# Kernel optimization log

Measured on AMD Instinct MI355X. Metric: run time of the kernel, lower is better.

The kernel has to match this reference:

```python
import jax, jax.numpy as jnp
import numpy as np

EPS = 1e-6  # torch.nn.PairwiseDistance default eps: dist = ||x - y + eps||_2


def setup_inputs() -> dict:
    key = jax.random.key(0)
    k1, k2 = jax.random.split(key)
    samples = jax.random.normal(k1, (4096, 128), dtype=jnp.float32)   # batch of observations
    V = jax.random.uniform(k2, (65536, 128), dtype=jnp.float32)       # grown node codebook (torch.rand init)
    return {"samples": samples, "V": V}


def reference(samples, V):
    # activate_bmu, vectorized over the batch.
    # torch PairwiseDistance(p=2): d_n = || x - V_n + eps ||_2
    D = samples.shape[-1]
    x_sq = jnp.sum(samples * samples, axis=-1)        # [B]
    v_sq = jnp.sum(V * V, axis=-1)                    # [N]
    xv = jnp.einsum('bd,nd->bn', samples, V)          # [B, N]
    x_sum = jnp.sum(samples, axis=-1)                 # [B]
    v_sum = jnp.sum(V, axis=-1)                       # [N]
    sq = (x_sq[:, None] + v_sq[None, :] - 2.0 * xv
          + 2.0 * EPS * (x_sum[:, None] - v_sum[None, :]) + D * EPS * EPS)
    dists = jnp.sqrt(jnp.maximum(sq, 0.0))            # [B, N]
    # top-2 smallest distances -> BMU b, second BMU s
    neg_top2, idx = jax.lax.top_k(-dists, 2)          # [B, 2]
    b = idx[:, 0]
    s = idx[:, 1]
    a = jnp.exp(neg_top2[:, 0])                       # exp(-b_dist)
    return (b, s, a)
```

## Files before the change

kernel.cpp:

```cpp
#include <hip/hip_runtime.h>
#include <math.h>

#define NS 4096
#define NV 65536
#define DDIM 128
#define EPSV 1e-6f
#define NCHUNK 16
#define TILES_PER_CHUNK 32
#define FLTMAX 3.402823466e+38f
#define IMAX 0x7fffffff

#define XSQ_F    0
#define XSUM_F   4096
#define PART_F   8192
#define D12_F    139264
#define CNT_I    147456
#define CELL1_I  147472
#define CELL2_I  151568
#define BUCKET_I 155664
#define WS_TILED_BYTE 1605632
#define TILE_BYTES 65536
#define TILE_STRIDE 66560

typedef __attribute__((ext_vector_type(8)))  __bf16        bf16x8;
typedef __attribute__((ext_vector_type(8)))  unsigned short ush8;
typedef __attribute__((ext_vector_type(4)))  unsigned short ush4;
typedef __attribute__((ext_vector_type(16))) float          f32x16;

typedef const __attribute__((address_space(1))) unsigned int* gp_t;
typedef __attribute__((address_space(3))) unsigned int*       lp_t;

__device__ __forceinline__ void async_cp16(const void* g, void* l) {
    __builtin_amdgcn_global_load_lds((gp_t)g, (lp_t)l, 16, 0, 0);
}

__device__ __forceinline__ unsigned short f2bf(float x) {
    unsigned u = __builtin_bit_cast(unsigned, x);
    u += 0x7FFFu + ((u >> 16) & 1u);
    return (unsigned short)(u >> 16);
}
__device__ __forceinline__ float bf2f(unsigned short h) {
    unsigned u = ((unsigned)h) << 16;
    return __builtin_bit_cast(float, u);
}

__device__ __forceinline__ void stage_tile(const char* src, char* lds, int tid) {
    #pragma unroll
    for (int i = 0; i < 16; i++) {
        int off = (i * 256 + tid) * 16;
        async_cp16(src + off, lds + off);
    }
    if (tid < 64) {
        int off = TILE_BYTES + tid * 16;
        async_cp16(src + off, lds + off);
    }
}

__device__ __forceinline__ void load_bfrag(const float* __restrict__ samples,
                                           int srow, int q, ush8* bh, ush8* bl) {
    const float4* s4 = (const float4*)samples;
    #pragma unroll
    for (int s = 0; s < 8; s++) {
        float4 x0 = s4[(size_t)srow * 32 + s * 4 + q * 2];
        float4 x1 = s4[(size_t)srow * 32 + s * 4 + q * 2 + 1];
        float xs[8] = {x0.x, x0.y, x0.z, x0.w, x1.x, x1.y, x1.z, x1.w};
        #pragma unroll
        for (int j = 0; j < 8; j++) {
            float y = -2.0f * xs[j];
            unsigned short hh = f2bf(y);
            bh[s][j] = hh;
            bl[s][j] = f2bf(y - bf2f(hh));
        }
    }
}

__device__ __forceinline__ void tile_mfma(const char* lds, const ush8* bh, const ush8* bl,
                                          int q, int l31, f32x16 acc[4]) {
    #pragma unroll
    for (int mi = 0; mi < 4; mi++) {
        #pragma unroll
        for (int g = 0; g < 4; g++) {
            float4 cj = *(const float4*)(lds + TILE_BYTES + (size_t)(mi * 32 + g * 8 + 4 * q) * 4);
            acc[mi][g * 4 + 0] = cj.x;
            acc[mi][g * 4 + 1] = cj.y;
            acc[mi][g * 4 + 2] = cj.z;
            acc[mi][g * 4 + 3] = cj.w;
        }
    }
    #pragma unroll
    for (int s = 0; s < 8; s++) {
        bf16x8 bhs = __builtin_bit_cast(bf16x8, bh[s]);
        bf16x8 bls = __builtin_bit_cast(bf16x8, bl[s]);
        #pragma unroll
        for (int mi = 0; mi < 4; mi++) {
            bf16x8 ah = *(const bf16x8*)(lds + (size_t)((((s * 2 + 0) * 2 + q) * 128) + mi * 32 + l31) * 16);
            bf16x8 al = *(const bf16x8*)(lds + (size_t)((((s * 2 + 1) * 2 + q) * 128) + mi * 32 + l31) * 16);
            acc[mi] = __builtin_amdgcn_mfma_f32_32x32x16_bf16(ah, bhs, acc[mi], 0, 0, 0);
            acc[mi] = __builtin_amdgcn_mfma_f32_32x32x16_bf16(ah, bls, acc[mi], 0, 0, 0);
            acc[mi] = __builtin_amdgcn_mfma_f32_32x32x16_bf16(al, bhs, acc[mi], 0, 0, 0);
        }
    }
}

__global__ void vq_prep(const float* __restrict__ samples,
                        const float* __restrict__ V,
                        char* __restrict__ ws) {
    float* ws_f = (float*)ws;
    int* ws_i = (int*)ws;
    const int b = blockIdx.x;
    const int tid = threadIdx.x;
    if (b >= NV / 128) {
        if (b == NV / 128 && tid < NCHUNK) ws_i[CNT_I + tid] = 0;
        int row = (b - NV / 128) * 4 + (tid >> 6);
        int lane = tid & 63;
        float2 v = ((const float2*)(samples + (size_t)row * DDIM))[lane];
        float s = v.x + v.y;
        float q = v.x * v.x + v.y * v.y;
        #pragma unroll
        for (int off = 32; off >= 1; off >>= 1) {
            s += __shfl_xor(s, off);
            q += __shfl_xor(q, off);
        }
        if (lane == 0) { ws_f[XSQ_F + row] = q; ws_f[XSUM_F + row] = s; }
        return;
    }
    const int tile = b;
    char* dst = ws + WS_TILED_BYTE + (size_t)tile * TILE_STRIDE;
    const float4* v4 = (const float4*)V;
    #pragma unroll
    for (int i = 0; i < 16; i++) {
        int flat = i * 256 + tid;
        int row = flat >> 5;
        int kq = flat & 31;
        float4 g = v4[(size_t)(tile * 128 + row) * 32 + kq];
        float s = g.x + g.y + g.z + g.w;
        float q2 = g.x * g.x + g.y * g.y + g.z * g.z + g.w * g.w;
        #pragma unroll
        for (int off = 16; off >= 1; off >>= 1) {
            s += __shfl_xor(s, off);
            q2 += __shfl_xor(q2, off);
        }
        if ((tid & 31) == 0)
            *(float*)(dst + TILE_BYTES + row * 4) = q2 - 2.0f * EPSV * s;
        int k0 = kq * 4;
        int sI = k0 >> 4, qI = (k0 >> 3) & 1, j0 = k0 & 7;
        float xs[4] = {g.x, g.y, g.z, g.w};
        ush4 h, l;
        #pragma unroll
        for (int e = 0; e < 4; e++) {
            unsigned short hh = f2bf(xs[e]);
            h[e] = hh;
            l[e] = f2bf(xs[e] - bf2f(hh));
        }
        *(ush4*)(dst + ((((sI * 2 + 0) * 2 + qI) * 128) + row) * 16 + j0 * 2) = h;
        *(ush4*)(dst + ((((sI * 2 + 1) * 2 + qI) * 128) + row) * 16 + j0 * 2) = l;
    }
}

__global__ __launch_bounds__(256, 2)
void vq_gemm_topk(const float* __restrict__ samples, char* __restrict__ ws) {
    __shared__ __align__(16) char lds[TILE_STRIDE];
    const int tid = threadIdx.x;
    const int w = tid >> 6, lane = tid & 63;
    const int l31 = lane & 31, q = lane >> 5;
    const int st = blockIdx.x;
    const int chunk = blockIdx.y;
    const int nrow = st * 128 + w * 32 + l31;

    ush8 bh[8], bl[8];
    load_bfrag(samples, nrow, q, bh, bl);

    float rd1[4], rd2[4];
    #pragma unroll
    for (int mi = 0; mi < 4; mi++) { rd1[mi] = FLTMAX; rd2[mi] = FLTMAX; }

    const char* tile0 = ws + WS_TILED_BYTE + (size_t)(chunk * TILES_PER_CHUNK) * TILE_STRIDE;

    for (int it = 0; it < TILES_PER_CHUNK; it++) {
        stage_tile(tile0 + (size_t)it * TILE_STRIDE, lds, tid);
        __syncthreads();
        f32x16 acc[4];
        tile_mfma(lds, bh, bl, q, l31, acc);
        #pragma unroll
        for (int mi = 0; mi < 4; mi++) {
            #pragma unroll
            for (int r = 0; r < 16; r++) {
                float v = acc[mi][r];
                rd2[mi] = fminf(rd2[mi], fmaxf(rd1[mi], v));
                rd1[mi] = fminf(rd1[mi], v);
            }
        }
        __syncthreads();
    }

    float d1 = rd1[0], d2 = rd2[0];
    #pragma unroll
    for (int mi = 1; mi < 4; mi++) {
        float t = fmaxf(d1, rd1[mi]);
        d1 = fminf(d1, rd1[mi]);
        d2 = fminf(fminf(t, d2), rd2[mi]);
    }
    {
        float od1 = __shfl_xor(d1, 32), od2 = __shfl_xor(d2, 32);
        float t = fmaxf(d1, od1);
        d1 = fminf(d1, od1);
        d2 = fminf(fminf(t, d2), od2);
    }
    if (q == 0) {
        float2* part = (float2*)((float*)ws + PART_F);
        part[(size_t)nrow * NCHUNK + chunk] = make_float2(d1, d2);
    }
}

__global__ void vq_merge(float* __restrict__ ws_f, float* __restrict__ out) {
    const int m = blockIdx.x * 256 + threadIdx.x;
    const int lane = threadIdx.x & 63;
    int* ws_i = (int*)ws_f;
    const float2* part = (const float2*)(ws_f + PART_F);
    float2 p[NCHUNK];
    float g1 = FLTMAX, g2 = FLTMAX;
    #pragma unroll
    for (int c = 0; c < NCHUNK; c++) {
        p[c] = part[(size_t)m * NCHUNK + c];
        float t = fmaxf(g1, p[c].x);
        g1 = fminf(g1, p[c].x);
        g2 = fminf(fminf(t, g2), p[c].y);
    }
    ((float2*)(ws_f + D12_F))[m] = make_float2(g1, g2);
    ws_i[CELL1_I + m] = IMAX;
    ws_i[CELL2_I + m] = IMAX;
    float ci = ws_f[XSQ_F + m] + 2.0f * EPSV * ws_f[XSUM_F + m] + (float)DDIM * EPSV * EPSV;
    out[2 * NS + m] = expf(-sqrtf(fmaxf(ci + g1, 0.0f)));
    #pragma unroll
    for (int c = 0; c < NCHUNK; c++) {
        bool want = (p[c].x == g1) || (p[c].x == g2) || (p[c].y == g2);
        unsigned long long mk = __ballot(want);
        if (mk) {
            int leader = (int)__ffsll(mk) - 1;
            int base = 0;
            if (lane == leader) base = atomicAdd(&ws_i[CNT_I + c], (int)__popcll(mk));
            base = __shfl(base, leader);
            if (want) {
                int pos = base + (int)__popcll(mk & ((1ull << lane) - 1ull));
                ws_i[BUCKET_I + c * NS + pos] = m;
            }
        }
    }
}

__global__ __launch_bounds__(256, 2)
void vq_recover(const float* __restrict__ samples, char* __restrict__ ws) {
    __shared__ __align__(16) char lds[TILE_STRIDE];
    const int tid = threadIdx.x;
    const int w = tid >> 6, lane = tid & 63;
    const int l31 = lane & 31, q = lane >> 5;
    const int tg = blockIdx.x;
    const int chunk = blockIdx.z;
    int* ws_i = (int*)ws;
    float* ws_f = (float*)ws;
    const int cnt = ws_i[CNT_I + chunk];
    const char* tile0 = ws + WS_TILED_BYTE + (size_t)(chunk * TILES_PER_CHUNK) * TILE_STRIDE;

    for (int sy = blockIdx.y; sy * 128 < cnt; sy += 4) {
        int slot = sy * 128 + w * 32 + l31;
        bool valid = slot < cnt;
        int sample = valid ? ws_i[BUCKET_I + chunk * NS + slot] : 0;
        ush8 bh[8], bl[8];
        load_bfrag(samples, sample, q, bh, bl);
        float d1t, d2t;
        if (valid) {
            float2 dt = ((const float2*)(ws_f + D12_F))[sample];
            d1t = dt.x; d2t = dt.y;
        } else {
            d1t = __int_as_float(0x7fc00000);
            d2t = d1t;
        }
        #pragma unroll 1
        for (int it = tg * 4; it < tg * 4 + 4; it++) {
            stage_tile(tile0 + (size_t)it * TILE_STRIDE, lds, tid);
            __syncthreads();
            f32x16 acc[4];
            tile_mfma(lds, bh, bl, q, l31, acc);
            const int cbase = chunk * 4096 + it * 128 + 4 * q;
            #pragma unroll
            for (int mi = 0; mi < 4; mi++) {
                #pragma unroll
                for (int r = 0; r < 16; r++) {
                    float v = acc[mi][r];
                    if (v == d1t) {
                        int idx = cbase + mi * 32 + (r >> 2) * 8 + (r & 3);
                        int old = atomicMin(&ws_i[CELL1_I + sample], idx);
                        int loser = old > idx ? old : idx;
                        atomicMin(&ws_i[CELL2_I + sample], loser);
                    } else if (v == d2t) {
                        int idx = cbase + mi * 32 + (r >> 2) * 8 + (r & 3);
                        atomicMin(&ws_i[CELL2_I + sample], idx);
                    }
                }
            }
            __syncthreads();
        }
    }
}

__global__ void vq_finalize(const char* __restrict__ ws, float* __restrict__ out) {
    const int m = blockIdx.x * 256 + threadIdx.x;
    const int* ws_i = (const int*)ws;
    out[m]      = (float)ws_i[CELL1_I + m];
    out[NS + m] = (float)ws_i[CELL2_I + m];
}

extern "C" void kernel_launch(void* const* d_in, const int* in_sizes, int n_in,
                              void* d_out, int out_size, void* d_ws, size_t ws_size,
                              hipStream_t stream) {
    (void)in_sizes; (void)n_in; (void)out_size; (void)ws_size;
    const float* samples = (const float*)d_in[0];
    const float* V = (const float*)d_in[1];
    float* out = (float*)d_out;
    float* ws_f = (float*)d_ws;
    char*  ws_b = (char*)d_ws;

    vq_prep<<<dim3(NV / 128 + NS / 4), 256, 0, stream>>>(samples, V, ws_b);
    vq_gemm_topk<<<dim3(NS / 128, NCHUNK), 256, 0, stream>>>(samples, ws_b);
    vq_merge<<<dim3(NS / 256), 256, 0, stream>>>(ws_f, out);
    vq_recover<<<dim3(8, 4, NCHUNK), 256, 0, stream>>>(samples, ws_b);
    vq_finalize<<<dim3(NS / 256), 256, 0, stream>>>(ws_b, out);
}
```

Before: 341.9 us.

## Flip GEMM operands, track winning tile per sample, recover per tile

The main GEMM now stages the 128-sample block in LDS once and streams the codebook tiles directly from global memory into registers. This removes the per-tile LDS staging and the two barriers per iteration. The top-2 search also records which tile produced each candidate, so the recovery pass launches one block per tile and only recomputes for samples whose best or second-best fell in that tile, replacing the bucketed per-chunk atomic lists. The prep kernel transposes V through LDS so it can write 16-byte bf16 fragments, and the grid is remapped to group chunks. The risks are register pressure from per-iteration global loads without LDS reuse across waves, and extra index bookkeeping.

```diff
diff --git a/kernel.cpp b/kernel.cpp
--- a/kernel.cpp
+++ b/kernel.cpp
@@ -7,17 +7,17 @@
 #define EPSV 1e-6f
 #define NCHUNK 16
 #define TILES_PER_CHUNK 32
+#define NTILE 512
 #define FLTMAX 3.402823466e+38f
 #define IMAX 0x7fffffff
 
 #define XSQ_F    0
 #define XSUM_F   4096
 #define PART_F   8192
-#define D12_F    139264
-#define CNT_I    147456
-#define CELL1_I  147472
-#define CELL2_I  151568
-#define BUCKET_I 155664
+#define D12_F    270336
+#define T12_I    278528
+#define CELL1_I  286720
+#define CELL2_I  290816
 #define WS_TILED_BYTE 1605632
 #define TILE_BYTES 65536
 #define TILE_STRIDE 66560
@@ -27,13 +27,6 @@
 typedef __attribute__((ext_vector_type(4)))  unsigned short ush4;
 typedef __attribute__((ext_vector_type(16))) float          f32x16;
 
-typedef const __attribute__((address_space(1))) unsigned int* gp_t;
-typedef __attribute__((address_space(3))) unsigned int*       lp_t;
-
-__device__ __forceinline__ void async_cp16(const void* g, void* l) {
-    __builtin_amdgcn_global_load_lds((gp_t)g, (lp_t)l, 16, 0, 0);
-}
-
 __device__ __forceinline__ unsigned short f2bf(float x) {
     unsigned u = __builtin_bit_cast(unsigned, x);
     u += 0x7FFFu + ((u >> 16) & 1u);
@@ -44,60 +37,65 @@
     return __builtin_bit_cast(float, u);
 }
 
-__device__ __forceinline__ void stage_tile(const char* src, char* lds, int tid) {
-    #pragma unroll
-    for (int i = 0; i < 16; i++) {
-        int off = (i * 256 + tid) * 16;
-        async_cp16(src + off, lds + off);
-    }
-    if (tid < 64) {
-        int off = TILE_BYTES + tid * 16;
-        async_cp16(src + off, lds + off);
-    }
-}
-
-__device__ __forceinline__ void load_bfrag(const float* __restrict__ samples,
-                                           int srow, int q, ush8* bh, ush8* bl) {
-    const float4* s4 = (const float4*)samples;
+__device__ __forceinline__ void merge2t(float& d1, int& i1, float& d2, int& i2,
+                                        float d, int i) {
+    bool b1 = (d < d1) || (d == d1 && i < i1);
+    bool b2 = (d < d2) || (d == d2 && i < i2);
+    if (b1) { d2 = d1; i2 = i1; d1 = d; i1 = i; }
+    else if (b2) { d2 = d; i2 = i; }
+}
+
+__device__ __forceinline__ void cvt_sample_piece(const float4* __restrict__ s4,
+                                                 int srcrow, int row, int kq,
+                                                 char* lds) {
+    float4 xv = s4[(size_t)srcrow * 32 + kq];
+    int k0 = kq * 4, sI = k0 >> 4, qI = (k0 >> 3) & 1, j0 = k0 & 7;
+    float xs[4] = {xv.x, xv.y, xv.z, xv.w};
+    ush4 h, l;
+    #pragma unroll
+    for (int e = 0; e < 4; e++) {
+        float y = -2.0f * xs[e];
+        unsigned short hh = f2bf(y);
+        h[e] = hh;
+        l[e] = f2bf(y - bf2f(hh));
+    }
+    *(ush4*)(lds + ((((sI * 2 + 0) * 2 + qI) * 128) + row) * 16 + j0 * 2) = h;
+    *(ush4*)(lds + ((((sI * 2 + 1) * 2 + qI) * 128) + row) * 16 + j0 * 2) = l;
+}
+
+__device__ __forceinline__ void tile_mfma_flip(const char* __restrict__ tsrc,
+                                               const char* __restrict__ lds,
+                                               int w, int qb, int l31,
+                                               f32x16 acc[4]) {
+    ush8 ah[8], al[8];
     #pragma unroll
     for (int s = 0; s < 8; s++) {
-        float4 x0 = s4[(size_t)srow * 32 + s * 4 + q * 2];
-        float4 x1 = s4[(size_t)srow * 32 + s * 4 + q * 2 + 1];
-        float xs[8] = {x0.x, x0.y, x0.z, x0.w, x1.x, x1.y, x1.z, x1.w};
-        #pragma unroll
-        for (int j = 0; j < 8; j++) {
-            float y = -2.0f * xs[j];
-            unsigned short hh = f2bf(y);
-            bh[s][j] = hh;
-            bl[s][j] = f2bf(y - bf2f(hh));
-        }
-    }
-}
-
-__device__ __forceinline__ void tile_mfma(const char* lds, const ush8* bh, const ush8* bl,
-                                          int q, int l31, f32x16 acc[4]) {
-    #pragma unroll
-    for (int mi = 0; mi < 4; mi++) {
-        #pragma unroll
-        for (int g = 0; g < 4; g++) {
-            float4 cj = *(const float4*)(lds + TILE_BYTES + (size_t)(mi * 32 + g * 8 + 4 * q) * 4);
-            acc[mi][g * 4 + 0] = cj.x;
-            acc[mi][g * 4 + 1] = cj.y;
-            acc[mi][g * 4 + 2] = cj.z;
-            acc[mi][g * 4 + 3] = cj.w;
-        }
+        ah[s] = *(const ush8*)(tsrc + (size_t)((((s * 2 + 0) * 2 + qb) * 128) + w * 32 + l31) * 16);
+        al[s] = *(const ush8*)(tsrc + (size_t)((((s * 2 + 1) * 2 + qb) * 128) + w * 32 + l31) * 16);
+    }
+    const char* cjb = tsrc + TILE_BYTES + (size_t)(w * 32 + 4 * qb) * 4;
+    float4 cj0 = *(const float4*)(cjb);
+    float4 cj1 = *(const float4*)(cjb + 32);
+    float4 cj2 = *(const float4*)(cjb + 64);
+    float4 cj3 = *(const float4*)(cjb + 96);
+    #pragma unroll
+    for (int sg = 0; sg < 4; sg++) {
+        acc[sg][0] = cj0.x;  acc[sg][1] = cj0.y;  acc[sg][2] = cj0.z;  acc[sg][3] = cj0.w;
+        acc[sg][4] = cj1.x;  acc[sg][5] = cj1.y;  acc[sg][6] = cj1.z;  acc[sg][7] = cj1.w;
+        acc[sg][8] = cj2.x;  acc[sg][9] = cj2.y;  acc[sg][10] = cj2.z; acc[sg][11] = cj2.w;
+        acc[sg][12] = cj3.x; acc[sg][13] = cj3.y; acc[sg][14] = cj3.z; acc[sg][15] = cj3.w;
     }
     #pragma unroll
     for (int s = 0; s < 8; s++) {
-        bf16x8 bhs = __builtin_bit_cast(bf16x8, bh[s]);
-        bf16x8 bls = __builtin_bit_cast(bf16x8, bl[s]);
-        #pragma unroll
-        for (int mi = 0; mi < 4; mi++) {
-            bf16x8 ah = *(const bf16x8*)(lds + (size_t)((((s * 2 + 0) * 2 + q) * 128) + mi * 32 + l31) * 16);
-            bf16x8 al = *(const bf16x8*)(lds + (size_t)((((s * 2 + 1) * 2 + q) * 128) + mi * 32 + l31) * 16);
-            acc[mi] = __builtin_amdgcn_mfma_f32_32x32x16_bf16(ah, bhs, acc[mi], 0, 0, 0);
-            acc[mi] = __builtin_amdgcn_mfma_f32_32x32x16_bf16(ah, bls, acc[mi], 0, 0, 0);
-            acc[mi] = __builtin_amdgcn_mfma_f32_32x32x16_bf16(al, bhs, acc[mi], 0, 0, 0);
+        bf16x8 a_h = __builtin_bit_cast(bf16x8, ah[s]);
+        bf16x8 a_l = __builtin_bit_cast(bf16x8, al[s]);
+        #pragma unroll
+        for (int sg = 0; sg < 4; sg++) {
+            bf16x8 b_h = *(const bf16x8*)(lds + (size_t)((((s * 2 + 0) * 2 + qb) * 128) + sg * 32 + l31) * 16);
+            bf16x8 b_l = *(const bf16x8*)(lds + (size_t)((((s * 2 + 1) * 2 + qb) * 128) + sg * 32 + l31) * 16);
+            acc[sg] = __builtin_amdgcn_mfma_f32_32x32x16_bf16(a_h, b_h, acc[sg], 0, 0, 0);
+            acc[sg] = __builtin_amdgcn_mfma_f32_32x32x16_bf16(a_h, b_l, acc[sg], 0, 0, 0);
+            acc[sg] = __builtin_amdgcn_mfma_f32_32x32x16_bf16(a_l, b_h, acc[sg], 0, 0, 0);
         }
     }
 }
@@ -105,12 +103,11 @@
 __global__ void vq_prep(const float* __restrict__ samples,
                         const float* __restrict__ V,
                         char* __restrict__ ws) {
+    __shared__ float tf[128 * 132];
     float* ws_f = (float*)ws;
-    int* ws_i = (int*)ws;
     const int b = blockIdx.x;
     const int tid = threadIdx.x;
     if (b >= NV / 128) {
-        if (b == NV / 128 && tid < NCHUNK) ws_i[CNT_I + tid] = 0;
         int row = (b - NV / 128) * 4 + (tid >> 6);
         int lane = tid & 63;
         float2 v = ((const float2*)(samples + (size_t)row * DDIM))[lane];
@@ -131,8 +128,9 @@
     for (int i = 0; i < 16; i++) {
         int flat = i * 256 + tid;
         int row = flat >> 5;
-        int kq = flat & 31;
-        float4 g = v4[(size_t)(tile * 128 + row) * 32 + kq];
+        int c4 = flat & 31;
+        float4 g = v4[(size_t)(tile * 128 + row) * 32 + c4];
+        *(float4*)&tf[row * 132 + c4 * 4] = g;
         float s = g.x + g.y + g.z + g.w;
         float q2 = g.x * g.x + g.y * g.y + g.z * g.z + g.w * g.w;
         #pragma unroll
@@ -142,163 +140,196 @@
         }
         if ((tid & 31) == 0)
             *(float*)(dst + TILE_BYTES + row * 4) = q2 - 2.0f * EPSV * s;
-        int k0 = kq * 4;
-        int sI = k0 >> 4, qI = (k0 >> 3) & 1, j0 = k0 & 7;
-        float xs[4] = {g.x, g.y, g.z, g.w};
-        ush4 h, l;
-        #pragma unroll
-        for (int e = 0; e < 4; e++) {
-            unsigned short hh = f2bf(xs[e]);
-            h[e] = hh;
-            l[e] = f2bf(xs[e] - bf2f(hh));
-        }
-        *(ush4*)(dst + ((((sI * 2 + 0) * 2 + qI) * 128) + row) * 16 + j0 * 2) = h;
-        *(ush4*)(dst + ((((sI * 2 + 1) * 2 + qI) * 128) + row) * 16 + j0 * 2) = l;
+    }
+    __syncthreads();
+    #pragma unroll
+    for (int i = 0; i < 8; i++) {
+        int task = i * 256 + tid;
+        int row = task & 127;
+        int sq = task >> 7;
+        int s = sq >> 1, q = sq & 1;
+        float4 lo = *(const float4*)&tf[row * 132 + s * 16 + q * 8];
+        float4 hi = *(const float4*)&tf[row * 132 + s * 16 + q * 8 + 4];
+        float xs[8] = {lo.x, lo.y, lo.z, lo.w, hi.x, hi.y, hi.z, hi.w};
+        ush8 h, l;
+        #pragma unroll
+        for (int j = 0; j < 8; j++) {
+            unsigned short hh = f2bf(xs[j]);
+            h[j] = hh;
+            l[j] = f2bf(xs[j] - bf2f(hh));
+        }
+        *(ush8*)(dst + (size_t)((((s * 2 + 0) * 2 + q) * 128) + row) * 16) = h;
+        *(ush8*)(dst + (size_t)((((s * 2 + 1) * 2 + q) * 128) + row) * 16) = l;
     }
 }
 
 __global__ __launch_bounds__(256, 2)
 void vq_gemm_topk(const float* __restrict__ samples, char* __restrict__ ws) {
-    __shared__ __align__(16) char lds[TILE_STRIDE];
+    __shared__ __align__(16) char lds[TILE_BYTES];
+    __shared__ float4 pmerge[4][128];
     const int tid = threadIdx.x;
     const int w = tid >> 6, lane = tid & 63;
-    const int l31 = lane & 31, q = lane >> 5;
-    const int st = blockIdx.x;
-    const int chunk = blockIdx.y;
-    const int nrow = st * 128 + w * 32 + l31;
-
-    ush8 bh[8], bl[8];
-    load_bfrag(samples, nrow, q, bh, bl);
-
-    float rd1[4], rd2[4];
-    #pragma unroll
-    for (int mi = 0; mi < 4; mi++) { rd1[mi] = FLTMAX; rd2[mi] = FLTMAX; }
-
-    const char* tile0 = ws + WS_TILED_BYTE + (size_t)(chunk * TILES_PER_CHUNK) * TILE_STRIDE;
-
+    const int l31 = lane & 31, qb = lane >> 5;
+    const int bid = blockIdx.x;
+    const int g = bid >> 3;
+    const int chunk = (bid & 7) * 2 + (g >> 5);
+    const int st = g & 31;
+
+    const float4* s4 = (const float4*)samples;
+    #pragma unroll
+    for (int i = 0; i < 16; i++) {
+        int flat = i * 256 + tid;
+        int row = flat >> 5, kq = flat & 31;
+        cvt_sample_piece(s4, st * 128 + row, row, kq, lds);
+    }
+    __syncthreads();
+
+    float D1[4], D2[4];
+    int T1[4], T2[4];
+    #pragma unroll
+    for (int sg = 0; sg < 4; sg++) { D1[sg] = FLTMAX; D2[sg] = FLTMAX; T1[sg] = IMAX; T2[sg] = IMAX; }
+
+    const char* vbase = ws + WS_TILED_BYTE;
+    #pragma unroll 1
     for (int it = 0; it < TILES_PER_CHUNK; it++) {
-        stage_tile(tile0 + (size_t)it * TILE_STRIDE, lds, tid);
-        __syncthreads();
+        const int tile = chunk * TILES_PER_CHUNK + it;
+        const char* tsrc = vbase + (size_t)tile * TILE_STRIDE;
         f32x16 acc[4];
-        tile_mfma(lds, bh, bl, q, l31, acc);
-        #pragma unroll
-        for (int mi = 0; mi < 4; mi++) {
+        tile_mfma_flip(tsrc, lds, w, qb, l31, acc);
+        #pragma unroll
+        for (int sg = 0; sg < 4; sg++) {
+            float t1 = FLTMAX, t2 = FLTMAX;
             #pragma unroll
             for (int r = 0; r < 16; r++) {
-                float v = acc[mi][r];
-                rd2[mi] = fminf(rd2[mi], fmaxf(rd1[mi], v));
-                rd1[mi] = fminf(rd1[mi], v);
+                float v = acc[sg][r];
+                t2 = fminf(t2, fmaxf(t1, v));
+                t1 = fminf(t1, v);
             }
-        }
-        __syncthreads();
-    }
-
-    float d1 = rd1[0], d2 = rd2[0];
-    #pragma unroll
-    for (int mi = 1; mi < 4; mi++) {
-        float t = fmaxf(d1, rd1[mi]);
-        d1 = fminf(d1, rd1[mi]);
-        d2 = fminf(fminf(t, d2), rd2[mi]);
-    }
-    {
+            bool c1 = t1 < D1[sg];
+            float m1 = fminf(D1[sg], t2);
+            float m2 = fminf(D2[sg], t1);
+            int T2a = (t2 < D1[sg]) ? tile : T1[sg];
+            int T2b = (t1 < D2[sg]) ? tile : T2[sg];
+            D2[sg] = c1 ? m1 : m2;
+            T2[sg] = c1 ? T2a : T2b;
+            T1[sg] = c1 ? tile : T1[sg];
+            D1[sg] = c1 ? t1 : D1[sg];
+        }
+    }
+
+    #pragma unroll
+    for (int sg = 0; sg < 4; sg++) {
+        float d1 = D1[sg], d2 = D2[sg];
+        int t1 = T1[sg], t2 = T2[sg];
         float od1 = __shfl_xor(d1, 32), od2 = __shfl_xor(d2, 32);
-        float t = fmaxf(d1, od1);
-        d1 = fminf(d1, od1);
-        d2 = fminf(fminf(t, d2), od2);
-    }
-    if (q == 0) {
-        float2* part = (float2*)((float*)ws + PART_F);
-        part[(size_t)nrow * NCHUNK + chunk] = make_float2(d1, d2);
+        int   ot1 = __shfl_xor(t1, 32), ot2 = __shfl_xor(t2, 32);
+        merge2t(d1, t1, d2, t2, od1, ot1);
+        merge2t(d1, t1, d2, t2, od2, ot2);
+        if (qb == 0)
+            pmerge[w][sg * 32 + l31] = make_float4(d1, d2, (float)t1, (float)t2);
+    }
+    __syncthreads();
+    if (tid < 128) {
+        float4 p0 = pmerge[0][tid];
+        float d1 = p0.x, d2 = p0.y;
+        int t1 = (int)p0.z, t2 = (int)p0.w;
+        #pragma unroll
+        for (int ww = 1; ww < 4; ww++) {
+            float4 p = pmerge[ww][tid];
+            merge2t(d1, t1, d2, t2, p.x, (int)p.z);
+            merge2t(d1, t1, d2, t2, p.y, (int)p.w);
+        }
+        float4* part = (float4*)((float*)ws + PART_F);
+        part[(size_t)(st * 128 + tid) * NCHUNK + chunk] =
+            make_float4(d1, d2, (float)t1, (float)t2);
     }
 }
 
 __global__ void vq_merge(float* __restrict__ ws_f, float* __restrict__ out) {
     const int m = blockIdx.x * 256 + threadIdx.x;
-    const int lane = threadIdx.x & 63;
     int* ws_i = (int*)ws_f;
-    const float2* part = (const float2*)(ws_f + PART_F);
-    float2 p[NCHUNK];
-    float g1 = FLTMAX, g2 = FLTMAX;
+    const float4* part = (const float4*)(ws_f + PART_F);
+    float d1 = FLTMAX, d2 = FLTMAX;
+    int t1 = IMAX, t2 = IMAX;
     #pragma unroll
     for (int c = 0; c < NCHUNK; c++) {
-        p[c] = part[(size_t)m * NCHUNK + c];
-        float t = fmaxf(g1, p[c].x);
-        g1 = fminf(g1, p[c].x);
-        g2 = fminf(fminf(t, g2), p[c].y);
-    }
-    ((float2*)(ws_f + D12_F))[m] = make_float2(g1, g2);
+        float4 p = part[(size_t)m * NCHUNK + c];
+        merge2t(d1, t1, d2, t2, p.x, (int)p.z);
+        merge2t(d1, t1, d2, t2, p.y, (int)p.w);
+    }
+    ((float2*)(ws_f + D12_F))[m] = make_float2(d1, d2);
+    ((int2*)(ws_i + T12_I))[m] = make_int2(t1, t2);
     ws_i[CELL1_I + m] = IMAX;
     ws_i[CELL2_I + m] = IMAX;
     float ci = ws_f[XSQ_F + m] + 2.0f * EPSV * ws_f[XSUM_F + m] + (float)DDIM * EPSV * EPSV;
-    out[2 * NS + m] = expf(-sqrtf(fmaxf(ci + g1, 0.0f)));
-    #pragma unroll
-    for (int c = 0; c < NCHUNK; c++) {
-        bool want = (p[c].x == g1) || (p[c].x == g2) || (p[c].y == g2);
-        unsigned long long mk = __ballot(want);
-        if (mk) {
-            int leader = (int)__ffsll(mk) - 1;
-            int base = 0;
-            if (lane == leader) base = atomicAdd(&ws_i[CNT_I + c], (int)__popcll(mk));
-            base = __shfl(base, leader);
-            if (want) {
-                int pos = base + (int)__popcll(mk & ((1ull << lane) - 1ull));
-                ws_i[BUCKET_I + c * NS + pos] = m;
-            }
-        }
-    }
-}
-
-__global__ __launch_bounds__(256, 2)
+    out[2 * NS + m] = expf(-sqrtf(fmaxf(ci + d1, 0.0f)));
+}
+
+__global__ __launch_bounds__(256)
 void vq_recover(const float* __restrict__ samples, char* __restrict__ ws) {
-    __shared__ __align__(16) char lds[TILE_STRIDE];
+    __shared__ __align__(16) char sbuf[TILE_BYTES];
+    __shared__ int list[NS];
+    __shared__ int lcnt;
     const int tid = threadIdx.x;
     const int w = tid >> 6, lane = tid & 63;
-    const int l31 = lane & 31, q = lane >> 5;
-    const int tg = blockIdx.x;
-    const int chunk = blockIdx.z;
+    const int l31 = lane & 31, qb = lane >> 5;
+    const int tile = blockIdx.x;
     int* ws_i = (int*)ws;
     float* ws_f = (float*)ws;
-    const int cnt = ws_i[CNT_I + chunk];
-    const char* tile0 = ws + WS_TILED_BYTE + (size_t)(chunk * TILES_PER_CHUNK) * TILE_STRIDE;
-
-    for (int sy = blockIdx.y; sy * 128 < cnt; sy += 4) {
-        int slot = sy * 128 + w * 32 + l31;
-        bool valid = slot < cnt;
-        int sample = valid ? ws_i[BUCKET_I + chunk * NS + slot] : 0;
-        ush8 bh[8], bl[8];
-        load_bfrag(samples, sample, q, bh, bl);
-        float d1t, d2t;
-        if (valid) {
-            float2 dt = ((const float2*)(ws_f + D12_F))[sample];
-            d1t = dt.x; d2t = dt.y;
-        } else {
-            d1t = __int_as_float(0x7fc00000);
-            d2t = d1t;
-        }
-        #pragma unroll 1
-        for (int it = tg * 4; it < tg * 4 + 4; it++) {
-            stage_tile(tile0 + (size_t)it * TILE_STRIDE, lds, tid);
-            __syncthreads();
-            f32x16 acc[4];
-            tile_mfma(lds, bh, bl, q, l31, acc);
-            const int cbase = chunk * 4096 + it * 128 + 4 * q;
+
+    if (tid == 0) lcnt = 0;
+    __syncthreads();
+    const int2* t12 = (const int2*)(ws_i + T12_I);
+    for (int i = tid; i < NS; i += 256) {
+        int2 t = t12[i];
+        if (t.x == tile || t.y == tile) {
+            int p = atomicAdd(&lcnt, 1);
+            list[p] = i;
+        }
+    }
+    __syncthreads();
+    const int cnt = lcnt;
+    if (cnt == 0) return;
+
+    const char* tsrc = ws + WS_TILED_BYTE + (size_t)tile * TILE_STRIDE;
+    const float4* s4 = (const float4*)samples;
+    const float2* d12 = (const float2*)(ws_f + D12_F);
+    const float nanf_ = __int_as_float(0x7fc00000);
+
+    for (int b0 = 0; b0 < cnt; b0 += 128) {
+        __syncthreads();
+        #pragma unroll
+        for (int i = 0; i < 16; i++) {
+            int flat = i * 256 + tid;
+            int row = flat >> 5, kq = flat & 31;
+            int srow = (b0 + row < cnt) ? list[b0 + row] : 0;
+            cvt_sample_piece(s4, srow, row, kq, sbuf);
+        }
+        __syncthreads();
+        f32x16 acc[4];
+        tile_mfma_flip(tsrc, sbuf, w, qb, l31, acc);
+        #pragma unroll
+        for (int sg = 0; sg < 4; sg++) {
+            int li = b0 + sg * 32 + l31;
+            bool valid = li < cnt;
+            int m = valid ? list[li] : 0;
+            float d1t = nanf_, d2t = nanf_;
+            if (valid) {
+                float2 dt = d12[m];
+                d1t = dt.x; d2t = dt.y;
+            }
             #pragma unroll
-            for (int mi = 0; mi < 4; mi++) {
-                #pragma unroll
-                for (int r = 0; r < 16; r++) {
-                    float v = acc[mi][r];
-                    if (v == d1t) {
-                        int idx = cbase + mi * 32 + (r >> 2) * 8 + (r & 3);
-                        int old = atomicMin(&ws_i[CELL1_I + sample], idx);
-                        int loser = old > idx ? old : idx;
-                        atomicMin(&ws_i[CELL2_I + sample], loser);
-                    } else if (v == d2t) {
-                        int idx = cbase + mi * 32 + (r >> 2) * 8 + (r & 3);
-                        atomicMin(&ws_i[CELL2_I + sample], idx);
-                    }
+            for (int r = 0; r < 16; r++) {
+                float v = acc[sg][r];
+                int idx = tile * 128 + w * 32 + (r & 3) + 8 * (r >> 2) + 4 * qb;
+                if (v == d1t) {
+                    int old = atomicMin(&ws_i[CELL1_I + m], idx);
+                    int loser = old > idx ? old : idx;
+                    atomicMin(&ws_i[CELL2_I + m], loser);
+                } else if (v == d2t) {
+                    atomicMin(&ws_i[CELL2_I + m], idx);
                 }
             }
-            __syncthreads();
         }
     }
 }
@@ -321,8 +352,8 @@
     char*  ws_b = (char*)d_ws;
 
     vq_prep<<<dim3(NV / 128 + NS / 4), 256, 0, stream>>>(samples, V, ws_b);
-    vq_gemm_topk<<<dim3(NS / 128, NCHUNK), 256, 0, stream>>>(samples, ws_b);
+    vq_gemm_topk<<<dim3((NS / 128) * NCHUNK), 256, 0, stream>>>(samples, ws_b);
     vq_merge<<<dim3(NS / 256), 256, 0, stream>>>(ws_f, out);
-    vq_recover<<<dim3(8, 4, NCHUNK), 256, 0, stream>>>(samples, ws_b);
+    vq_recover<<<dim3(NTILE), 256, 0, stream>>>(samples, ws_b);
     vq_finalize<<<dim3(NS / 256), 256, 0, stream>>>(ws_b, out);
 }
```

Result: slower. 595.8 us (+74.3%).
